# Kernel optimization log

Hardware: AMD Instinct MI355X
Metric: run time of the kernel (lower is better)

The kernel has to match this reference:

```python
import jax, jax.numpy as jnp
import numpy as np

B, S, D, H = 2, 2048, 1024, 16
DH = D // H

def setup_inputs() -> dict:
    key = jax.random.key(0)
    k1, k2, k3, k4 = jax.random.split(key, 4)
    x = jax.random.normal(k1, (B, S, D), dtype=jnp.float32)
    # flax Dense kernels: [in_features, out_features]
    w_qkv = jax.random.normal(k2, (D, 3 * D), dtype=jnp.float32) / np.sqrt(D)
    w_out = jax.random.normal(k3, (D, D), dtype=jnp.float32) / np.sqrt(D)
    b_out = jax.random.normal(k4, (D,), dtype=jnp.float32) * 0.01
    return {"x": x, "w_qkv": w_qkv, "w_out": w_out, "b_out": b_out}

def reference(x, w_qkv, w_out, b_out):
    b, s, d = x.shape
    h, dh = H, d // H
    qkv = jnp.einsum('bsd,de->bse', x, w_qkv)           # [B,S,3D]
    qkv = qkv.reshape(b, s, 3, h, dh)
    qkv = jnp.transpose(qkv, (2, 0, 3, 1, 4))            # [3,B,H,S,DH]
    q, k, v = qkv[0], qkv[1], qkv[2]
    attn = jnp.einsum('bhqd,bhkd->bhqk', q, k) / jnp.sqrt(jnp.float32(dh))
    attn = jax.nn.softmax(attn, axis=-1)                 # [B,H,S,S]
    y = jnp.einsum('bhqk,bhkd->bhqd', attn, v)           # [B,H,S,DH]
    y = jnp.transpose(y, (0, 2, 1, 3)).reshape(b, s, d)  # [B,S,D]
    return jnp.einsum('bsd,de->bse', y, w_out) + b_out
```

## Files before the change

kernel.cpp:

```cpp
#include <hip/hip_runtime.h>
#include <stdint.h>

typedef __bf16 bf16_t;
typedef __bf16 bf16x8 __attribute__((ext_vector_type(8)));
typedef float f32x4 __attribute__((ext_vector_type(4)));
typedef float f32x16 __attribute__((ext_vector_type(16)));
typedef unsigned short u16;
typedef unsigned short u16x4 __attribute__((ext_vector_type(4)));
typedef unsigned short u16x8 __attribute__((ext_vector_type(8)));
typedef unsigned int u32;
typedef unsigned int u32x4 __attribute__((ext_vector_type(4)));

#define DEVI __device__ __forceinline__


DEVI u16 bits(float f) { bf16_t h = (bf16_t)f; return __builtin_bit_cast(u16, h); }

DEVI void gld16(const void* g, void* l) {
  __builtin_amdgcn_global_load_lds(
      (const __attribute__((address_space(1))) unsigned int*)g,
      (__attribute__((address_space(3))) unsigned int*)l, 16, 0, 0);
}

DEVI bf16x8 ldsr(const u16* s, int row, int cg) {
  const int byte = row * 128 + ((cg ^ (row & 7)) << 4);
  return *(const bf16x8*)((const char*)s + byte);
}

DEVI bf16x8 ldsrV(const u16* s, int row, int cg) {
  const int byte = row * 256 + ((cg ^ (row & 15)) << 4);
  return *(const bf16x8*)((const char*)s + byte);
}

DEVI float exp2v(float x) { return __builtin_amdgcn_exp2f(x); }

DEVI u32 cvtpk(float lo, float hi) {
  u32 r;
  asm("v_cvt_pk_bf16_f32 %0, %1, %2" : "=v"(r) : "v"(lo), "v"(hi));
  return r;
}

#define MFMA16(a, b, c) __builtin_amdgcn_mfma_f32_16x16x32_bf16(a, b, c, 0, 0, 0)
#define MFMA32(a, b, c) __builtin_amdgcn_mfma_f32_32x32x16_bf16(a, b, c, 0, 0, 0)

#define MKFRAG(dst, S, B)                                              \
  {                                                                    \
    u32 a_ = cvtpk(S[(B) + 0], S[(B) + 1]);                            \
    u32 b_ = cvtpk(S[(B) + 4], S[(B) + 5]);                            \
    u32 c_ = cvtpk(S[(B) + 2], S[(B) + 3]);                            \
    u32 d_ = cvtpk(S[(B) + 6], S[(B) + 7]);                            \
    asm("v_permlane32_swap_b32 %0, %1" : "+v"(a_), "+v"(b_));          \
    asm("v_permlane32_swap_b32 %0, %1" : "+v"(c_), "+v"(d_));          \
    u32x4 u_ = {a_, c_, b_, d_};                                       \
    dst = __builtin_bit_cast(bf16x8, u_);                              \
  }

__global__ void __launch_bounds__(256) cvt8(const float* __restrict__ in,
                                            u16* __restrict__ out, int n8) {
  const int i = blockIdx.x * 256 + threadIdx.x;
  if (i >= n8) return;
  const f32x4* p = (const f32x4*)in;
  const f32x4 a = p[2 * i], b = p[2 * i + 1];
  u16x8 o;
#pragma unroll
  for (int j = 0; j < 4; ++j) { o[j] = bits(a[j]); o[4 + j] = bits(b[j]); }
  *(u16x8*)(out + (size_t)i * 8) = o;
}

__global__ void __launch_bounds__(256) tconv2(const float* __restrict__ wqkv,
                                              const float* __restrict__ wout,
                                              u16* __restrict__ oqkv,
                                              u16* __restrict__ oout) {
  __shared__ float T[64][65];
  const int K = 1024;
  const int sel = blockIdx.y >= 48;
  const float* in = sel ? wout : wqkv;
  u16* out = sel ? oout : oqkv;
  const int N = sel ? 1024 : 3072;
  const int k0 = blockIdx.x * 64, n0 = (sel ? blockIdx.y - 48 : blockIdx.y) * 64;
  const int tid = threadIdx.x;
#pragma unroll
  for (int i = 0; i < 4; ++i) {
    const int c = i * 256 + tid;
    const int row = c >> 4, c4 = c & 15;
    const f32x4 v = *(const f32x4*)(in + (size_t)(k0 + row) * N + n0 + c4 * 4);
#pragma unroll
    for (int j = 0; j < 4; ++j) T[row][c4 * 4 + j] = v[j];
  }
  __syncthreads();
#pragma unroll
  for (int i = 0; i < 2; ++i) {
    const int c = i * 256 + tid;
    const int nrow = c >> 3, k8 = c & 7;
    u16x8 o;
#pragma unroll
    for (int j = 0; j < 8; ++j) o[j] = bits(T[k8 * 8 + j][nrow]);
    *(u16x8*)(out + (size_t)(n0 + nrow) * K + k0 + k8 * 8) = o;
  }
}

template <int BN>
DEVI void gemm_core(const u16* __restrict__ A, const u16* __restrict__ Bt,
                    u16* As, u16* Bs, int m0, int n0, int Kdim,
                    f32x4 (&acc)[4][BN / 32]) {
  const int NF = BN / 32;
  const int tid = threadIdx.x;
  const int l = tid & 63, w = tid >> 6;
  const int lr = l & 15, lh = l >> 4;
  const int wr = w >> 1, wc = w & 1;
  for (int kt = 0; kt < Kdim; kt += 64) {
#pragma unroll
    for (int i = 0; i < 4; ++i) {
      const int cb = i * 256 + w * 64;
      const int c = cb + l;
      const int row = c >> 3;
      const int col = ((c & 7) ^ (row & 7)) << 3;
      gld16(A + (size_t)(m0 + row) * Kdim + kt + col, As + (size_t)cb * 8);
    }
#pragma unroll
    for (int i = 0; i < BN / 32; ++i) {
      const int cb = i * 256 + w * 64;
      const int c = cb + l;
      const int row = c >> 3;
      const int col = ((c & 7) ^ (row & 7)) << 3;
      gld16(Bt + (size_t)(n0 + row) * Kdim + kt + col, Bs + (size_t)cb * 8);
    }
    __syncthreads();
#pragma unroll
    for (int kk = 0; kk < 2; ++kk) {
      bf16x8 af[4], bfr[NF];
#pragma unroll
      for (int m = 0; m < 4; ++m) af[m] = ldsr(As, wr * 64 + m * 16 + lr, kk * 4 + lh);
#pragma unroll
      for (int n = 0; n < NF; ++n)
        bfr[n] = ldsr(Bs, wc * (BN / 2) + n * 16 + lr, kk * 4 + lh);
#pragma unroll
      for (int m = 0; m < 4; ++m)
#pragma unroll
        for (int n = 0; n < NF; ++n)
          acc[m][n] = MFMA16(af[m], bfr[n], acc[m][n]);
    }
    __syncthreads();
  }
}


DEVI void stage_half(const u16* __restrict__ G, int row0, int kt, u16* dst) {
  const int tid = threadIdx.x;
  const int l = tid & 63, wv = tid >> 6;
  const u16* gp = G + (size_t)row0 * 1024 + kt;
#pragma unroll
  for (int i = 0; i < 2; ++i) {
    const int cb = i * 512 + wv * 64;
    const int c = cb + l;
    const int rih = c >> 3;
    const int col = ((c & 7) ^ (rih & 7)) << 3;
    gld16(gp + (size_t)rih * 1024 + col, dst + cb * 8);
  }
}

template <bool SA1, bool SB2, int VM>
DEVI void qkv_tile(const u16* __restrict__ A, const u16* __restrict__ Bt,
                   int m0, int n0, int ktA1, int ktB2,
                   u16* Ac, u16* Bc, u16* An, f32x4 (&acc)[8][4]) {
  const int tid = threadIdx.x;
  const int l = tid & 63, wv = tid >> 6;
  const int lr = l & 15, lh = l >> 4;
  const int wr = wv >> 2, wc = wv & 3;
  const int ab = wr * 128, bb = wc * 64;
  bf16x8 a0[8], a1[8], b0[4], b1[4];
#pragma unroll
  for (int m = 0; m < 4; ++m)
#pragma unroll
    for (int kk = 0; kk < 2; ++kk)
      a0[m * 2 + kk] = ldsr(Ac, ab + m * 16 + lr, kk * 4 + lh);
#pragma unroll
  for (int n = 0; n < 2; ++n)
#pragma unroll
    for (int kk = 0; kk < 2; ++kk)
      b0[n * 2 + kk] = ldsr(Bc, bb + n * 16 + lr, kk * 4 + lh);
  if (SA1) stage_half(A, m0, ktA1, An);
  __builtin_amdgcn_s_barrier();
  asm volatile("s_waitcnt lgkmcnt(0)" ::: "memory");
  __builtin_amdgcn_sched_barrier(0);
  __builtin_amdgcn_s_setprio(1);
#pragma unroll
  for (int m = 0; m < 4; ++m)
#pragma unroll
    for (int n = 0; n < 2; ++n)
#pragma unroll
      for (int kk = 0; kk < 2; ++kk)
        acc[m][n] = MFMA16(a0[m * 2 + kk], b0[n * 2 + kk], acc[m][n]);
  __builtin_amdgcn_s_setprio(0);
  __builtin_amdgcn_s_barrier();
#pragma unroll
  for (int n = 0; n < 2; ++n)
#pragma unroll
    for (int kk = 0; kk < 2; ++kk)
      b1[n * 2 + kk] = ldsr(Bc, bb + 32 + n * 16 + lr, kk * 4 + lh);
  if (SA1) stage_half(A, m0 + 128, ktA1, An + 8192);
  __builtin_amdgcn_s_barrier();
  asm volatile("s_waitcnt lgkmcnt(0)" ::: "memory");
  __builtin_amdgcn_sched_barrier(0);
  __builtin_amdgcn_s_setprio(1);
#pragma unroll
  for (int m = 0; m < 4; ++m)
#pragma unroll
    for (int n = 0; n < 2; ++n)
#pragma unroll
      for (int kk = 0; kk < 2; ++kk)
        acc[m][2 + n] = MFMA16(a0[m * 2 + kk], b1[n * 2 + kk], acc[m][2 + n]);
  __builtin_amdgcn_s_setprio(0);
  __builtin_amdgcn_s_barrier();
#pragma unroll
  for (int m = 0; m < 4; ++m)
#pragma unroll
    for (int kk = 0; kk < 2; ++kk)
      a1[m * 2 + kk] = ldsr(Ac, ab + 64 + m * 16 + lr, kk * 4 + lh);
  if (SB2) stage_half(Bt, n0, ktB2, Bc);
  __builtin_amdgcn_s_barrier();
  asm volatile("s_waitcnt lgkmcnt(0)" ::: "memory");
  __builtin_amdgcn_sched_barrier(0);
  __builtin_amdgcn_s_setprio(1);
#pragma unroll
  for (int m = 0; m < 4; ++m)
#pragma unroll
    for (int n = 0; n < 2; ++n)
#pragma unroll
      for (int kk = 0; kk < 2; ++kk)
        acc[4 + m][n] = MFMA16(a1[m * 2 + kk], b0[n * 2 + kk], acc[4 + m][n]);
  __builtin_amdgcn_s_setprio(0);
  __builtin_amdgcn_s_barrier();
  if (SB2) stage_half(Bt, n0 + 128, ktB2, Bc + 8192);
  __builtin_amdgcn_s_barrier();
  __builtin_amdgcn_s_setprio(1);
#pragma unroll
  for (int m = 0; m < 4; ++m)
#pragma unroll
    for (int n = 0; n < 2; ++n)
#pragma unroll
      for (int kk = 0; kk < 2; ++kk)
        acc[4 + m][2 + n] = MFMA16(a1[m * 2 + kk], b1[n * 2 + kk], acc[4 + m][2 + n]);
  __builtin_amdgcn_s_setprio(0);
  if (VM == 4) asm volatile("s_waitcnt vmcnt(4)" ::: "memory");
  else if (VM == 0) asm volatile("s_waitcnt vmcnt(0)" ::: "memory");
  __builtin_amdgcn_s_barrier();
}

__global__ void __launch_bounds__(512, 2) gemm_qkv_k(const u16* __restrict__ A,
                                                     const u16* __restrict__ Bt,
                                                     u16* __restrict__ Qb,
                                                     u16* __restrict__ Kb,
                                                     u16* __restrict__ Vtb) {
  __shared__ u16 LA[2][16384], LB[2][16384];
  const int bid = blockIdx.x;
  const int g = bid & 7, w24 = bid >> 3;
  const int mt = (g >> 1) * 4 + (w24 & 3);
  const int nt = (g & 1) * 6 + (w24 >> 2);
  const int m0 = mt * 256, n0 = nt * 256;

  stage_half(A, m0, 0, LA[0]);
  stage_half(A, m0 + 128, 0, LA[0] + 8192);
  stage_half(Bt, n0, 0, LB[0]);
  stage_half(Bt, n0 + 128, 0, LB[0] + 8192);
  stage_half(Bt, n0, 64, LB[1]);
  stage_half(Bt, n0 + 128, 64, LB[1] + 8192);
  asm volatile("s_waitcnt vmcnt(4)" ::: "memory");
  __builtin_amdgcn_s_barrier();

  f32x4 acc[8][4] = {};
  u16 *Ac = LA[0], *Bc = LB[0], *An = LA[1], *Bn = LB[1];
#pragma unroll 1
  for (int t = 0; t < 14; ++t) {
    qkv_tile<true, true, 4>(A, Bt, m0, n0, (t + 1) * 64, (t + 2) * 64, Ac, Bc, An, acc);
    u16* tp = Ac; Ac = An; An = tp;
    tp = Bc; Bc = Bn; Bn = tp;
  }
  qkv_tile<true, false, 0>(A, Bt, m0, n0, 15 * 64, 0, Ac, Bc, An, acc);
  { u16* tp = Ac; Ac = An; An = tp; tp = Bc; Bc = Bn; Bn = tp; }
  qkv_tile<false, false, -1>(A, Bt, m0, n0, 0, 0, Ac, Bc, An, acc);

  const int tid = threadIdx.x;
  const int l = tid & 63, wv = tid >> 6;
  const int lr = l & 15, lh = l >> 4;
  const int wr = wv >> 2, wc = wv & 3;
  if (n0 >= 2048) {
    const int b = m0 >> 11, s0 = m0 & 2047;
#pragma unroll
    for (int n = 0; n < 4; ++n) {
      const int ng = n0 + wc * 64 + n * 16 + lr;
      const int h = (ng >> 6) & 15, dh = ng & 63;
      u16* vrow = Vtb + ((size_t)(b * 16 + h) * 64 + dh) * 2048 + s0;
#pragma unroll
      for (int m = 0; m < 8; ++m) {
        const int s = wr * 128 + m * 16 + lh * 4;
        u16x4 pk;
        pk[0] = bits(acc[m][n][0]);
        pk[1] = bits(acc[m][n][1]);
        pk[2] = bits(acc[m][n][2]);
        pk[3] = bits(acc[m][n][3]);
        *(u16x4*)(vrow + s) = pk;
      }
    }
  } else {
#pragma unroll
    for (int n = 0; n < 4; ++n) {
      const int ng = n0 + wc * 64 + n * 16 + lr;
      const int sel = ng >> 10, h = (ng >> 6) & 15, dh = ng & 63;
      u16* dst = sel == 0 ? Qb : Kb;
      const float qs = (sel == 0) ? 0.125f * 1.44269504f : 1.0f;
#pragma unroll
      for (int m = 0; m < 8; ++m) {
#pragma unroll
        for (int r = 0; r < 4; ++r) {
          const int mg = m0 + wr * 128 + m * 16 + lh * 4 + r;
          const int b = mg >> 11, s = mg & 2047;
          dst[((size_t)(b * 16 + h) * 2048 + s) * 64 + dh] = bits(acc[m][n][r] * qs);
        }
      }
    }
  }
}

__global__ void __launch_bounds__(256) gemm_out_k(const u16* __restrict__ A,
                                                  const u16* __restrict__ Bt,
                                                  const float* __restrict__ bias,
                                                  float* __restrict__ out) {
  __shared__ u16 As[128 * 64], Bs[128 * 64];
  const int m0 = blockIdx.y * 128, n0 = blockIdx.x * 128;
  f32x4 acc[4][4] = {};
  gemm_core<128>(A, Bt, As, Bs, m0, n0, 1024, acc);
  const int tid = threadIdx.x;
  const int l = tid & 63, w = tid >> 6;
  const int lr = l & 15, lh = l >> 4;
  const int wr = w >> 1, wc = w & 1;
#pragma unroll
  for (int n = 0; n < 4; ++n) {
    const int ng = n0 + wc * 64 + n * 16 + lr;
    const float bv = bias[ng];
#pragma unroll
    for (int m = 0; m < 4; ++m) {
#pragma unroll
      for (int r = 0; r < 4; ++r) {
        const int mg = m0 + wr * 64 + m * 16 + lh * 4 + r;
        out[(size_t)mg * 1024 + ng] = acc[m][n][r] + bv;
      }
    }
  }
}

__global__ void __launch_bounds__(512, 4) attn_k(const u16* __restrict__ Qb,
                                                 const u16* __restrict__ Kb,
                                                 const u16* __restrict__ Vt,
                                                 u16* __restrict__ Yb) {
  __shared__ char smem[65536];
  u16* const KsA = (u16*)smem;
  u16* const KsB = (u16*)(smem + 16384);
  u16* const VsA = (u16*)(smem + 32768);
  u16* const VsB = (u16*)(smem + 49152);

  const int tid = threadIdx.x;
  const int l = tid & 63, w = tid >> 6;
  const int lq = l & 31, hi = l >> 5;
  const int qw = w & 3;
  const int khalf = w >> 2;
  const int i0 = blockIdx.x;
  const int bid = (i0 & 7) * 64 + (i0 >> 3);
  const int bh = bid >> 4, qt = bid & 15;

  const u16* Qp = Qb + ((size_t)bh * 2048 + qt * 128 + qw * 32 + lq) * 64;
  bf16x8 qf0 = *(const bf16x8*)(Qp + hi * 8);
  bf16x8 qf1 = *(const bf16x8*)(Qp + 16 + hi * 8);
  bf16x8 qf2 = *(const bf16x8*)(Qp + 32 + hi * 8);
  bf16x8 qf3 = *(const bf16x8*)(Qp + 48 + hi * 8);

  const u16* Kbase = Kb + (size_t)bh * 2048 * 64;
  const u16* Vbase = Vt + (size_t)bh * 64 * 2048;

  bf16x8 ones;
#pragma unroll
  for (int j = 0; j < 8; ++j) ones[j] = (bf16_t)1.0f;

  f32x16 acc0 = {}, acc1 = {};
  f32x16 accs = {};

#define STAGE(Ksb, Vsb, kv0)                                               \
  {                                                                        \
    _Pragma("unroll") for (int ii = 0; ii < 2; ++ii) {                     \
      const int cb = ii * 512 + w * 64;                                    \
      const int c = cb + l;                                                \
      const int krow = c >> 3;                                             \
      const int kcol = ((c & 7) ^ (krow & 7)) << 3;                        \
      gld16(Kbase + (size_t)((kv0) + krow) * 64 + kcol, (Ksb) + cb * 8);   \
      const int vrow = c >> 4;                                             \
      const int vcol = ((c & 15) ^ (vrow & 15)) << 3;                      \
      gld16(Vbase + (size_t)vrow * 2048 + (kv0) + vcol, (Vsb) + cb * 8);   \
    }                                                                      \
  }

  STAGE(KsA, VsA, 0);
  asm volatile("s_waitcnt vmcnt(0)" ::: "memory");
  __builtin_amdgcn_s_barrier();

  bf16x8 pc0 = ones, pc1 = ones;
  int cur = 0;
#pragma unroll 1
  for (int t = 0; t < 16; ++t) {
    const u16* Ksc = cur ? KsB : KsA;
    const u16* Vsc = cur ? VsB : VsA;
    const u16* Vsp = cur ? VsA : VsB;

    if (t > 0) {
      __builtin_amdgcn_s_setprio(1);
      accs = MFMA32(pc0, ones, accs);
      acc0 = MFMA32(pc0, ldsrV(Vsp, lq, khalf * 8 + 4 + hi), acc0);
      acc1 = MFMA32(pc0, ldsrV(Vsp, 32 + lq, khalf * 8 + 4 + hi), acc1);
      accs = MFMA32(pc1, ones, accs);
      acc0 = MFMA32(pc1, ldsrV(Vsp, lq, khalf * 8 + 6 + hi), acc0);
      acc1 = MFMA32(pc1, ldsrV(Vsp, 32 + lq, khalf * 8 + 6 + hi), acc1);
      __builtin_amdgcn_s_setprio(0);
      asm volatile("s_waitcnt vmcnt(0)" ::: "memory");
      __builtin_amdgcn_s_barrier();
    }
    if (t + 1 < 16) STAGE((cur ? KsA : KsB), (cur ? VsA : VsB), (t + 1) * 128);

    f32x16 s0 = {}, s1 = {};
    __builtin_amdgcn_s_setprio(1);
    s0 = MFMA32(ldsr(Ksc, khalf * 64 + lq, hi), qf0, s0);
    s0 = MFMA32(ldsr(Ksc, khalf * 64 + lq, 2 + hi), qf1, s0);
    s0 = MFMA32(ldsr(Ksc, khalf * 64 + lq, 4 + hi), qf2, s0);
    s0 = MFMA32(ldsr(Ksc, khalf * 64 + lq, 6 + hi), qf3, s0);
    s1 = MFMA32(ldsr(Ksc, khalf * 64 + 32 + lq, hi), qf0, s1);
    s0[0] = exp2v(s0[0]); s0[1] = exp2v(s0[1]); s0[2] = exp2v(s0[2]); s0[3] = exp2v(s0[3]);
    s1 = MFMA32(ldsr(Ksc, khalf * 64 + 32 + lq, 2 + hi), qf1, s1);
    s0[4] = exp2v(s0[4]); s0[5] = exp2v(s0[5]); s0[6] = exp2v(s0[6]); s0[7] = exp2v(s0[7]);
    s1 = MFMA32(ldsr(Ksc, khalf * 64 + 32 + lq, 4 + hi), qf2, s1);
    s0[8] = exp2v(s0[8]); s0[9] = exp2v(s0[9]); s0[10] = exp2v(s0[10]); s0[11] = exp2v(s0[11]);
    s1 = MFMA32(ldsr(Ksc, khalf * 64 + 32 + lq, 6 + hi), qf3, s1);
    s0[12] = exp2v(s0[12]); s0[13] = exp2v(s0[13]); s0[14] = exp2v(s0[14]); s0[15] = exp2v(s0[15]);
    __builtin_amdgcn_s_setprio(0);

    bf16x8 pa0, pa1;
    MKFRAG(pa0, s0, 0);
    MKFRAG(pa1, s0, 8);

    __builtin_amdgcn_s_setprio(1);
    accs = MFMA32(pa0, ones, accs);
    s1[0] = exp2v(s1[0]); s1[1] = exp2v(s1[1]); s1[2] = exp2v(s1[2]);
    acc0 = MFMA32(pa0, ldsrV(Vsc, lq, khalf * 8 + hi), acc0);
    s1[3] = exp2v(s1[3]); s1[4] = exp2v(s1[4]); s1[5] = exp2v(s1[5]);
    acc1 = MFMA32(pa0, ldsrV(Vsc, 32 + lq, khalf * 8 + hi), acc1);
    s1[6] = exp2v(s1[6]); s1[7] = exp2v(s1[7]); s1[8] = exp2v(s1[8]);
    accs = MFMA32(pa1, ones, accs);
    s1[9] = exp2v(s1[9]); s1[10] = exp2v(s1[10]); s1[11] = exp2v(s1[11]);
    acc0 = MFMA32(pa1, ldsrV(Vsc, lq, khalf * 8 + 2 + hi), acc0);
    s1[12] = exp2v(s1[12]); s1[13] = exp2v(s1[13]); s1[14] = exp2v(s1[14]);
    acc1 = MFMA32(pa1, ldsrV(Vsc, 32 + lq, khalf * 8 + 2 + hi), acc1);
    s1[15] = exp2v(s1[15]);
    __builtin_amdgcn_s_setprio(0);

    MKFRAG(pc0, s1, 0);
    MKFRAG(pc1, s1, 8);
    cur ^= 1;
  }
  {
    const u16* Vsp = cur ? VsA : VsB;
    accs = MFMA32(pc0, ones, accs);
    acc0 = MFMA32(pc0, ldsrV(Vsp, lq, khalf * 8 + 4 + hi), acc0);
    acc1 = MFMA32(pc0, ldsrV(Vsp, 32 + lq, khalf * 8 + 4 + hi), acc1);
    accs = MFMA32(pc1, ones, accs);
    acc0 = MFMA32(pc1, ldsrV(Vsp, lq, khalf * 8 + 6 + hi), acc0);
    acc1 = MFMA32(pc1, ldsrV(Vsp, 32 + lq, khalf * 8 + 6 + hi), acc1);
  }
#undef STAGE
  __syncthreads();

  float* const F = (float*)smem;
  float* const Fp = F + (size_t)(tid & 255) * 49;
  if (khalf) {
#pragma unroll
    for (int r = 0; r < 16; ++r) {
      Fp[r] = acc0[r];
      Fp[16 + r] = acc1[r];
      Fp[32 + r] = accs[r];
    }
  }
  __syncthreads();
  if (khalf) return;
#pragma unroll
  for (int r = 0; r < 16; ++r) {
    acc0[r] += Fp[r];
    acc1[r] += Fp[16 + r];
    accs[r] += Fp[32 + r];
  }

  const int b = bh >> 4, h = bh & 15;
#pragma unroll
  for (int r = 0; r < 16; ++r) {
    const float sd = 1.0f / accs[r];
    const int row = (r & 3) + 8 * (r >> 2) + 4 * hi;
    const int sq = qt * 128 + qw * 32 + row;
    u16* yp = Yb + ((size_t)b * 2048 + sq) * 1024 + h * 64;
    yp[lq] = bits(acc0[r] * sd);
    yp[32 + lq] = bits(acc1[r] * sd);
  }
}

extern "C" void kernel_launch(void* const* d_in, const int* in_sizes, int n_in,
                              void* d_out, int out_size, void* d_ws, size_t ws_size,
                              hipStream_t stream) {
  (void)in_sizes; (void)n_in; (void)out_size; (void)ws_size;
  const float* x     = (const float*)d_in[0];
  const float* w_qkv = (const float*)d_in[1];
  const float* w_out = (const float*)d_in[2];
  const float* b_out = (const float*)d_in[3];
  float* out = (float*)d_out;

  char* ws = (char*)d_ws;
  u16* xb    = (u16*)(ws);
  u16* wqkvT = (u16*)(ws + 8388608);
  u16* woutT = (u16*)(ws + 14680064);
  u16* Qb    = (u16*)(ws + 16777216);
  u16* Kb    = (u16*)(ws + 25165824);
  u16* Vt    = (u16*)(ws + 41943040);
  u16* Yb    = xb;

  cvt8<<<2048, 256, 0, stream>>>(x, xb, 4194304 / 8);
  tconv2<<<dim3(16, 64), 256, 0, stream>>>(w_qkv, w_out, wqkvT, woutT);
  gemm_qkv_k<<<192, 512, 0, stream>>>(xb, wqkvT, Qb, Kb, Vt);
  attn_k<<<512, 512, 0, stream>>>(Qb, Kb, Vt, Yb);
  gemm_out_k<<<dim3(8, 32), 256, 0, stream>>>(Yb, woutT, b_out, out);
}
```

Before: 113.7 us.

## Compute softmax row sums with VALU adds and merge prep kernels into one launch

Drops the MFMA-with-ones trick for softmax denominators. Each lane now sums its exponentials in fp32 registers, combines the two half-wave partials with a permlane32 swap, and exchanges them across the two key halves through shared memory. This removes a third of the PV-phase MFMAs and a 16-register accumulator, at the cost of extra VALU adds and a small LDS exchange. Separately, the input conversion and weight transpose kernels are merged into one launch to save a kernel dispatch.

```diff
diff --git a/kernel.cpp b/kernel.cpp
--- a/kernel.cpp
+++ b/kernel.cpp
@@ -55,30 +55,32 @@
     dst = __builtin_bit_cast(bf16x8, u_);                              \
   }
 
-__global__ void __launch_bounds__(256) cvt8(const float* __restrict__ in,
-                                            u16* __restrict__ out, int n8) {
-  const int i = blockIdx.x * 256 + threadIdx.x;
-  if (i >= n8) return;
-  const f32x4* p = (const f32x4*)in;
-  const f32x4 a = p[2 * i], b = p[2 * i + 1];
-  u16x8 o;
-#pragma unroll
-  for (int j = 0; j < 4; ++j) { o[j] = bits(a[j]); o[4 + j] = bits(b[j]); }
-  *(u16x8*)(out + (size_t)i * 8) = o;
-}
-
-__global__ void __launch_bounds__(256) tconv2(const float* __restrict__ wqkv,
-                                              const float* __restrict__ wout,
-                                              u16* __restrict__ oqkv,
-                                              u16* __restrict__ oout) {
+__global__ void __launch_bounds__(256) prep(const float* __restrict__ x,
+                                            const float* __restrict__ wqkv,
+                                            const float* __restrict__ wout,
+                                            u16* __restrict__ xb,
+                                            u16* __restrict__ oqkv,
+                                            u16* __restrict__ oout) {
   __shared__ float T[64][65];
-  const int K = 1024;
-  const int sel = blockIdx.y >= 48;
+  const int bid = blockIdx.x;
+  const int tid = threadIdx.x;
+  if (bid < 2048) {
+    const int i = bid * 256 + tid;
+    const f32x4* p = (const f32x4*)x;
+    const f32x4 a = p[2 * i], b = p[2 * i + 1];
+    u16x8 o;
+#pragma unroll
+    for (int j = 0; j < 4; ++j) { o[j] = bits(a[j]); o[4 + j] = bits(b[j]); }
+    *(u16x8*)(xb + (size_t)i * 8) = o;
+    return;
+  }
+  const int rem = bid - 2048;
+  const int bx = rem & 15, byy = rem >> 4;
+  const int sel = byy >= 48;
   const float* in = sel ? wout : wqkv;
   u16* out = sel ? oout : oqkv;
   const int N = sel ? 1024 : 3072;
-  const int k0 = blockIdx.x * 64, n0 = (sel ? blockIdx.y - 48 : blockIdx.y) * 64;
-  const int tid = threadIdx.x;
+  const int k0 = bx * 64, n0 = (sel ? byy - 48 : byy) * 64;
 #pragma unroll
   for (int i = 0; i < 4; ++i) {
     const int c = i * 256 + tid;
@@ -95,7 +97,7 @@
     u16x8 o;
 #pragma unroll
     for (int j = 0; j < 8; ++j) o[j] = bits(T[k8 * 8 + j][nrow]);
-    *(u16x8*)(out + (size_t)(n0 + nrow) * K + k0 + k8 * 8) = o;
+    *(u16x8*)(out + (size_t)(n0 + nrow) * 1024 + k0 + k8 * 8) = o;
   }
 }
 
@@ -377,12 +379,8 @@
   const u16* Kbase = Kb + (size_t)bh * 2048 * 64;
   const u16* Vbase = Vt + (size_t)bh * 64 * 2048;
 
-  bf16x8 ones;
-#pragma unroll
-  for (int j = 0; j < 8; ++j) ones[j] = (bf16_t)1.0f;
-
   f32x16 acc0 = {}, acc1 = {};
-  f32x16 accs = {};
+  float ssum = 0.f;
 
 #define STAGE(Ksb, Vsb, kv0)                                               \
   {                                                                        \
@@ -402,7 +400,7 @@
   asm volatile("s_waitcnt vmcnt(0)" ::: "memory");
   __builtin_amdgcn_s_barrier();
 
-  bf16x8 pc0 = ones, pc1 = ones;
+  bf16x8 pc0 = {}, pc1 = {};
   int cur = 0;
 #pragma unroll 1
   for (int t = 0; t < 16; ++t) {
@@ -412,10 +410,8 @@
 
     if (t > 0) {
       __builtin_amdgcn_s_setprio(1);
-      accs = MFMA32(pc0, ones, accs);
       acc0 = MFMA32(pc0, ldsrV(Vsp, lq, khalf * 8 + 4 + hi), acc0);
       acc1 = MFMA32(pc0, ldsrV(Vsp, 32 + lq, khalf * 8 + 4 + hi), acc1);
-      accs = MFMA32(pc1, ones, accs);
       acc0 = MFMA32(pc1, ldsrV(Vsp, lq, khalf * 8 + 6 + hi), acc0);
       acc1 = MFMA32(pc1, ldsrV(Vsp, 32 + lq, khalf * 8 + 6 + hi), acc1);
       __builtin_amdgcn_s_setprio(0);
@@ -443,46 +439,60 @@
     bf16x8 pa0, pa1;
     MKFRAG(pa0, s0, 0);
     MKFRAG(pa1, s0, 8);
+    {
+      const float q01 = (s0[0] + s0[1]) + (s0[2] + s0[3]);
+      const float q23 = (s0[4] + s0[5]) + (s0[6] + s0[7]);
+      const float q45 = (s0[8] + s0[9]) + (s0[10] + s0[11]);
+      const float q67 = (s0[12] + s0[13]) + (s0[14] + s0[15]);
+      ssum += (q01 + q23) + (q45 + q67);
+    }
 
     __builtin_amdgcn_s_setprio(1);
-    accs = MFMA32(pa0, ones, accs);
-    s1[0] = exp2v(s1[0]); s1[1] = exp2v(s1[1]); s1[2] = exp2v(s1[2]);
     acc0 = MFMA32(pa0, ldsrV(Vsc, lq, khalf * 8 + hi), acc0);
-    s1[3] = exp2v(s1[3]); s1[4] = exp2v(s1[4]); s1[5] = exp2v(s1[5]);
+    s1[0] = exp2v(s1[0]); s1[1] = exp2v(s1[1]); s1[2] = exp2v(s1[2]); s1[3] = exp2v(s1[3]);
     acc1 = MFMA32(pa0, ldsrV(Vsc, 32 + lq, khalf * 8 + hi), acc1);
-    s1[6] = exp2v(s1[6]); s1[7] = exp2v(s1[7]); s1[8] = exp2v(s1[8]);
-    accs = MFMA32(pa1, ones, accs);
-    s1[9] = exp2v(s1[9]); s1[10] = exp2v(s1[10]); s1[11] = exp2v(s1[11]);
+    s1[4] = exp2v(s1[4]); s1[5] = exp2v(s1[5]); s1[6] = exp2v(s1[6]); s1[7] = exp2v(s1[7]);
     acc0 = MFMA32(pa1, ldsrV(Vsc, lq, khalf * 8 + 2 + hi), acc0);
-    s1[12] = exp2v(s1[12]); s1[13] = exp2v(s1[13]); s1[14] = exp2v(s1[14]);
+    s1[8] = exp2v(s1[8]); s1[9] = exp2v(s1[9]); s1[10] = exp2v(s1[10]); s1[11] = exp2v(s1[11]);
     acc1 = MFMA32(pa1, ldsrV(Vsc, 32 + lq, khalf * 8 + 2 + hi), acc1);
-    s1[15] = exp2v(s1[15]);
+    s1[12] = exp2v(s1[12]); s1[13] = exp2v(s1[13]); s1[14] = exp2v(s1[14]); s1[15] = exp2v(s1[15]);
     __builtin_amdgcn_s_setprio(0);
 
     MKFRAG(pc0, s1, 0);
     MKFRAG(pc1, s1, 8);
+    {
+      const float q01 = (s1[0] + s1[1]) + (s1[2] + s1[3]);
+      const float q23 = (s1[4] + s1[5]) + (s1[6] + s1[7]);
+      const float q45 = (s1[8] + s1[9]) + (s1[10] + s1[11]);
+      const float q67 = (s1[12] + s1[13]) + (s1[14] + s1[15]);
+      ssum += (q01 + q23) + (q45 + q67);
+    }
     cur ^= 1;
   }
   {
     const u16* Vsp = cur ? VsA : VsB;
-    accs = MFMA32(pc0, ones, accs);
     acc0 = MFMA32(pc0, ldsrV(Vsp, lq, khalf * 8 + 4 + hi), acc0);
     acc1 = MFMA32(pc0, ldsrV(Vsp, 32 + lq, khalf * 8 + 4 + hi), acc1);
-    accs = MFMA32(pc1, ones, accs);
     acc0 = MFMA32(pc1, ldsrV(Vsp, lq, khalf * 8 + 6 + hi), acc0);
     acc1 = MFMA32(pc1, ldsrV(Vsp, 32 + lq, khalf * 8 + 6 + hi), acc1);
   }
 #undef STAGE
+
+  u32 sa = __builtin_bit_cast(u32, ssum), sb = sa;
+  asm("v_permlane32_swap_b32 %0, %1" : "+v"(sa), "+v"(sb));
+  const float tot = __builtin_bit_cast(float, sa) + __builtin_bit_cast(float, sb);
+
   __syncthreads();
 
   float* const F = (float*)smem;
   float* const Fp = F + (size_t)(tid & 255) * 49;
+  float* const F2 = (float*)(smem + 50176);
+  if (l < 32) F2[khalf * 128 + qw * 32 + l] = tot;
   if (khalf) {
 #pragma unroll
     for (int r = 0; r < 16; ++r) {
       Fp[r] = acc0[r];
       Fp[16 + r] = acc1[r];
-      Fp[32 + r] = accs[r];
     }
   }
   __syncthreads();
@@ -491,14 +501,13 @@
   for (int r = 0; r < 16; ++r) {
     acc0[r] += Fp[r];
     acc1[r] += Fp[16 + r];
-    accs[r] += Fp[32 + r];
   }
 
   const int b = bh >> 4, h = bh & 15;
 #pragma unroll
   for (int r = 0; r < 16; ++r) {
-    const float sd = 1.0f / accs[r];
     const int row = (r & 3) + 8 * (r >> 2) + 4 * hi;
+    const float sd = 1.0f / (F2[qw * 32 + row] + F2[128 + qw * 32 + row]);
     const int sq = qt * 128 + qw * 32 + row;
     u16* yp = Yb + ((size_t)b * 2048 + sq) * 1024 + h * 64;
     yp[lq] = bits(acc0[r] * sd);
@@ -525,8 +534,7 @@
   u16* Vt    = (u16*)(ws + 41943040);
   u16* Yb    = xb;
 
-  cvt8<<<2048, 256, 0, stream>>>(x, xb, 4194304 / 8);
-  tconv2<<<dim3(16, 64), 256, 0, stream>>>(w_qkv, w_out, wqkvT, woutT);
+  prep<<<3072, 256, 0, stream>>>(x, w_qkv, w_out, xb, wqkvT, woutT);
   gemm_qkv_k<<<192, 512, 0, stream>>>(xb, wqkvT, Qb, Kb, Vt);
   attn_k<<<512, 512, 0, stream>>>(Qb, Kb, Vt, Yb);
   gemm_out_k<<<dim3(8, 32), 256, 0, stream>>>(Yb, woutT, b_out, out);
```

Result: slower. 117.6 us (+3.5%).
